# Kernel optimization log

Hardware: AMD Instinct MI355X
Metric: run time of the kernel (lower is better)

Reference implementation:

```python
import jax, jax.numpy as jnp
import numpy as np

REF_MIC = 0
LOAD = 0.001 / np.sqrt(2.0)  # diagonal loading added to both real and imag parts


def _to_complex(x):
    # x: (N, 2, ...) real/imag stacked -> complex (N, ...)
    return x[:, 0] + 1j * x[:, 1]


def setup_inputs() -> dict:
    key = jax.random.key(0)
    k1, k2, k3 = jax.random.split(key, 3)
    N, C, T, F = 8, 16, 300, 257
    mixture = jax.random.normal(k1, (N, 2, C, T, F), dtype=jnp.float32)
    target = jax.random.normal(k2, (N, 2, C, T, F), dtype=jnp.float32)
    steering_vector = jax.random.normal(k3, (N, 2, C, F), dtype=jnp.float32)
    return {"mixture": mixture, "target": target, "steering_vector": steering_vector}


def reference(mixture, target, steering_vector):
    N, _, C, T, F = mixture.shape
    y = _to_complex(mixture)  # (N, C, T, F)
    x = _to_complex(target)   # (N, C, T, F)

    # Spatial covariance of mixture, mean over time frames (sum/T), fused einsum
    # phi[n,f] = (1/T) * sum_t y[n,:,t,f] y[n,:,t,f]^H  -> (N, F, C, C)
    phi = jnp.einsum('nctf,ndtf->nfcd', y, jnp.conj(y)) / T
    eye = jnp.eye(C, dtype=phi.dtype)
    # original adds load to BOTH real and imag diagonals (broadcast over RI dim)
    phi = phi + (LOAD + 1j * LOAD) * eye
    phi_inv = jnp.linalg.inv(phi)  # (N, F, C, C)

    # Cross covariance between mixture and reference-mic target
    A = jnp.transpose(y, (0, 3, 2, 1))            # (N, F, T, C)
    b = jnp.transpose(x[:, REF_MIC], (0, 2, 1))   # (N, F, T)
    mu_a = jnp.mean(A, axis=(0, 2), keepdims=True)  # mean over batch and time
    mu_b = jnp.mean(b, axis=(0, 2), keepdims=True)
    # mean over T of (A-mu_a)(b-mu_b)^H -> (N, F, C)
    phi_yx0 = jnp.mean((A - mu_a) * jnp.conj(b - mu_b)[..., None], axis=2)

    # MWF weights: w = phi_inv @ phi_yx0  -> (N, F, C)
    w = jnp.einsum('nfcd,nfd->nfc', phi_inv, phi_yx0)

    # Beamform: X_bf[n,t,f] = w[n,f]^H y[n,:,t,f]
    Xbf = jnp.einsum('nfc,nctf->ntf', jnp.conj(w), y)  # (N, T, F)

    # Back to real/imag stacked (N, 2, 1, T, F) matching torch output layout
    out = jnp.stack([Xbf.real, Xbf.imag], axis=1)[:, :, None]
    return out
```

## Files before the change

### kernel.cpp

```cpp
#include <hip/hip_runtime.h>

#define N_     8
#define C_     16
#define T_     300
#define F_     257
#define TF_    (T_*F_)
#define CTF_   (C_*TF_)
#define N2CTF_ (2*CTF_)

#define FT_    32
#define NFT_   9
#define TS_    5
#define RST_   35
#define SROWS_ 88
#define SCNT_  (SROWS_*RST_)
#define NTILE_ 10
#define PHIC_  (NTILE_*16)

#define MREC_  272

#define LOADC  7.0710678118654755e-04f

typedef float v2f __attribute__((ext_vector_type(2)));

__device__ __forceinline__ float2 cmul(float2 a, float2 b) {
  return make_float2(a.x*b.x - a.y*b.y, a.x*b.y + a.y*b.x);
}
__device__ __forceinline__ float2 cmulc(float2 a, float2 b) {
  return make_float2(a.x*b.x + a.y*b.y, a.y*b.x - a.x*b.y);
}
__device__ __forceinline__ float2 cdiv(float2 a, float2 b) {
  float inv = 1.0f / (b.x*b.x + b.y*b.y);
  return make_float2((a.x*b.x + a.y*b.y)*inv, (a.y*b.x - a.x*b.y)*inv);
}
__device__ __forceinline__ float2 cadd(float2 a, float2 b){ return make_float2(a.x+b.x, a.y+b.y); }
__device__ __forceinline__ float2 csub(float2 a, float2 b){ return make_float2(a.x-b.x, a.y-b.y); }

template<int TCH>
__global__ __launch_bounds__(320, 1) void k1_cov(const float* __restrict__ mix,
                                                 const float* __restrict__ tgt,
                                                 float2* __restrict__ phi_pf,
                                                 float2* __restrict__ syx_pf,
                                                 float2* __restrict__ sy_pf,
                                                 float2* __restrict__ sx_pf) {
  __shared__ v2f ys[SCNT_];
  v2f* phi_p = (v2f*)phi_pf;
  v2f* syx_p = (v2f*)syx_pf;
  v2f* sy_p  = (v2f*)sy_pf;
  v2f* sx_p  = (v2f*)sx_pf;
  const int tid = threadIdx.x;
  const int ft = blockIdx.x, tc = blockIdx.y, n = blockIdx.z;
  const int fbase = ft * FT_;
  const int t0 = tc * TCH;
  const int fl = tid & 31;
  const int g  = tid >> 5;
  int ti = 0, tj = g;
  while (tj > ti) { ++ti; tj -= ti; }
  const int c0 = ti * 4;
  const int d0 = tj * 4;
  const bool sThread = (tj == 0);
  const bool xg = (g < 5);

  const float* mixN = mix + n * N2CTF_;
  const float* tgtN = tgt + n * N2CTF_;

  const int ts_g   = g >> 1;
  const int c_base = (g & 1) * 8;
  const int row0   = ts_g * 16 + c_base;
  const int f_ld = min(fbase + fl, F_ - 1);
  const float* ybase = mixN + c_base * TF_ + f_ld;
  const float* xbase = tgtN + f_ld;

  v2f acc[4][4];
  #pragma unroll
  for (int i = 0; i < 4; ++i)
    #pragma unroll
    for (int j = 0; j < 4; ++j) acc[i][j] = (v2f){0.f, 0.f};
  v2f syx[4], sy[4], sx = (v2f){0.f, 0.f};
  #pragma unroll
  for (int i = 0; i < 4; ++i) { syx[i] = (v2f){0.f,0.f}; sy[i] = (v2f){0.f,0.f}; }

  float lr[9], li[9];
  {
    #pragma unroll
    for (int k = 0; k < 8; ++k) {
      const float* p = ybase + k * TF_ + (t0 + ts_g) * F_;
      lr[k] = p[0]; li[k] = p[CTF_];
    }
    if (xg) { const float* p = xbase + (t0 + g) * F_; lr[8] = p[0]; li[8] = p[CTF_]; }
    #pragma unroll
    for (int k = 0; k < 8; ++k)
      ys[(row0 + k) * RST_ + fl] = (v2f){lr[k], li[k]};
    if (xg) ys[(80 + g) * RST_ + fl] = (v2f){lr[8], li[8]};
  }

  constexpr int NS = TCH / TS_;
  for (int stg = 0; stg < NS; ++stg) {
    __syncthreads();
    const bool more = (stg + 1 < NS);
    if (more) {
      const int tS = t0 + (stg + 1) * TS_;
      #pragma unroll
      for (int k = 0; k < 8; ++k) {
        const float* p = ybase + k * TF_ + (tS + ts_g) * F_;
        lr[k] = p[0]; li[k] = p[CTF_];
      }
      if (xg) { const float* p = xbase + (tS + g) * F_; lr[8] = p[0]; li[8] = p[CTF_]; }
    }
    #pragma unroll
    for (int tl = 0; tl < TS_; ++tl) {
      const int rb = tl * 16;
      v2f a[4], bu[4], bv[4];
      #pragma unroll
      for (int i = 0; i < 4; ++i) a[i] = ys[(rb + c0 + i) * RST_ + fl];
      #pragma unroll
      for (int j = 0; j < 4; ++j) {
        v2f b = ys[(rb + d0 + j) * RST_ + fl];
        bu[j] = (v2f){b.x, -b.y};
        bv[j] = (v2f){b.y,  b.x};
      }
      #pragma unroll
      for (int i = 0; i < 4; ++i)
        #pragma unroll
        for (int j = 0; j < 4; ++j)
          acc[i][j] += a[i].x * bu[j] + a[i].y * bv[j];
      if (sThread) {
        v2f xv = ys[(80 + tl) * RST_ + fl];
        v2f xu = (v2f){xv.x, -xv.y};
        v2f xw = (v2f){xv.y,  xv.x};
        #pragma unroll
        for (int i = 0; i < 4; ++i) {
          syx[i] += a[i].x * xu + a[i].y * xw;
          sy[i]  += a[i];
        }
        if (g == 0) sx += xv;
      }
    }
    __syncthreads();
    if (more) {
      #pragma unroll
      for (int k = 0; k < 8; ++k)
        ys[(row0 + k) * RST_ + fl] = (v2f){lr[k], li[k]};
      if (xg) ys[(80 + g) * RST_ + fl] = (v2f){lr[8], li[8]};
    }
  }

  const int f = fbase + fl;
  if (f < F_) {
    const int tcn = tc * N_ + n;
    v2f* pb = phi_p + ((size_t)tcn * F_ + f) * PHIC_ + g * 16;
    #pragma unroll
    for (int i = 0; i < 4; ++i)
      #pragma unroll
      for (int j = 0; j < 4; ++j) pb[i * 4 + j] = acc[i][j];
    if (sThread) {
      v2f* s1 = syx_p + ((size_t)tcn * F_ + f) * C_ + c0;
      v2f* s2 = sy_p  + ((size_t)tcn * F_ + f) * C_ + c0;
      #pragma unroll
      for (int i = 0; i < 4; ++i) { s1[i] = syx[i]; s2[i] = sy[i]; }
      if (g == 0) sx_p[(size_t)tcn * F_ + f] = sx;
    }
  }
}

template<int TCP>
__global__ __launch_bounds__(256) void k2a_reduce(const float2* __restrict__ phi_p,
                                                  const float2* __restrict__ syx_p,
                                                  const float2* __restrict__ sy_p,
                                                  const float2* __restrict__ sx_p,
                                                  float2* __restrict__ Mg) {
  __shared__ float2 ld_sy[TCP * N_ * C_];
  __shared__ float2 ld_syx[TCP * C_];
  __shared__ float2 ld_sx[TCP * N_];
  __shared__ float2 muB_s, sxO_s;
  const int f = blockIdx.x, n = blockIdx.y;
  const int tid = threadIdx.x;
  const int i = tid >> 4, j = tid & 15;

  const int ti = i >> 2, tj = j >> 2, ci = i & 3, cj = j & 3;
  int gL, cell; bool cj_flip;
  if (ti >= tj) { gL = ti * (ti + 1) / 2 + tj; cell = ci * 4 + cj; cj_flip = false; }
  else          { gL = tj * (tj + 1) / 2 + ti; cell = cj * 4 + ci; cj_flip = true; }
  const int off = gL * 16 + cell;

  float2 s = make_float2(0.f, 0.f);
  for (int tc = 0; tc < TCP; ++tc) {
    float2 v = phi_p[((size_t)(tc * N_ + n) * F_ + f) * PHIC_ + off];
    s.x += v.x; s.y += v.y;
  }
  if (cj_flip) s.y = -s.y;
  if (i == j) { s.x += (float)T_ * LOADC; s.y += (float)T_ * LOADC; }

  for (int idx = tid; idx < TCP * N_ * C_; idx += 256) {
    int tcn = idx >> 4, c = idx & 15;
    ld_sy[idx] = sy_p[((size_t)tcn * F_ + f) * C_ + c];
  }
  for (int idx = tid; idx < TCP * C_; idx += 256) {
    int tc = idx >> 4, c = idx & 15;
    ld_syx[idx] = syx_p[((size_t)(tc * N_ + n) * F_ + f) * C_ + c];
  }
  for (int idx = tid; idx < TCP * N_; idx += 256) {
    ld_sx[idx] = sx_p[(size_t)idx * F_ + f];
  }
  __syncthreads();

  float2 muA_r = make_float2(0.f,0.f), ownY = make_float2(0.f,0.f), ownYX = make_float2(0.f,0.f);
  if (tid < 16) {
    float2 allY = make_float2(0.f,0.f);
    for (int tcn = 0; tcn < TCP * N_; ++tcn) allY = cadd(allY, ld_sy[tcn * C_ + tid]);
    for (int tc = 0; tc < TCP; ++tc) {
      ownY  = cadd(ownY,  ld_sy[(tc * N_ + n) * C_ + tid]);
      ownYX = cadd(ownYX, ld_syx[tc * C_ + tid]);
    }
    const float invNT = 1.0f / ((float)N_ * (float)T_);
    muA_r = make_float2(allY.x * invNT, allY.y * invNT);
  }
  if (tid == 16) {
    float2 own = make_float2(0.f,0.f), all = make_float2(0.f,0.f);
    for (int tc = 0; tc < TCP; ++tc)
      for (int nn = 0; nn < N_; ++nn) {
        float2 v = ld_sx[tc * N_ + nn];
        all = cadd(all, v);
        if (nn == n) own = cadd(own, v);
      }
    const float invNT = 1.0f / ((float)N_ * (float)T_);
    muB_s = make_float2(all.x * invNT, all.y * invNT);
    sxO_s = own;
  }
  __syncthreads();

  float2* dst = Mg + (size_t)(n * F_ + f) * MREC_;
  dst[tid] = s;
  if (tid < 16) {
    float2 r = ownYX;
    r = csub(r, cmulc(muA_r, sxO_s));
    r = csub(r, cmulc(ownY, muB_s));
    float2 t3 = cmulc(muA_r, muB_s);
    r.x += (float)T_ * t3.x; r.y += (float)T_ * t3.y;
    dst[256 + tid] = r;
  }
}

__global__ __launch_bounds__(64) void k2b_solve(const float2* __restrict__ Mg,
                                                float* __restrict__ wre,
                                                float* __restrict__ wim) {
  __shared__ float2 M[16 * 17];
  const int f = blockIdx.x, n = blockIdx.y;
  const int tid = threadIdx.x;
  const float2* src = Mg + (size_t)(n * F_ + f) * MREC_;
  #pragma unroll
  for (int r = 0; r < 4; ++r) {
    int idx = tid + 64 * r;
    M[(idx >> 4) * 17 + (idx & 15)] = src[idx];
  }
  if (tid < 16) M[tid * 17 + 16] = src[256 + tid];
  __syncthreads();

  const int i = tid >> 2, q = tid & 3;
  for (int k = 0; k < 16; ++k) {
    float2 fac = cdiv(M[i * 17 + k], M[k * 17 + k]);
    __syncthreads();
    if (i != k) {
      #pragma unroll
      for (int jj = 0; jj < 4; ++jj) {
        int j = q * 4 + jj;
        M[i * 17 + j] = csub(M[i * 17 + j], cmul(fac, M[k * 17 + j]));
      }
      if (q == 3) M[i * 17 + 16] = csub(M[i * 17 + 16], cmul(fac, M[k * 17 + 16]));
    }
    __syncthreads();
  }
  if (q == 0) {
    float2 w = cdiv(M[i * 17 + 16], M[i * 17 + i]);
    wre[(n * C_ + i) * F_ + f] = w.x;
    wim[(n * C_ + i) * F_ + f] = w.y;
  }
}

__global__ __launch_bounds__(320) void k3_bf(const float* __restrict__ mix,
                                             const float* __restrict__ wre,
                                             const float* __restrict__ wim,
                                             float* __restrict__ out) {
  const int t0 = blockIdx.x * 2, n = blockIdx.y;
  const int f = threadIdx.x;
  if (f >= F_) return;
  const float* mixN = mix + n * N2CTF_;
  const float* wR = wre + n * C_ * F_;
  const float* wI = wim + n * C_ * F_;
  float* outN = out + n * 2 * TF_;
  float wr[16], wi[16];
  #pragma unroll
  for (int c = 0; c < 16; ++c) { wr[c] = wR[c * F_ + f]; wi[c] = wI[c * F_ + f]; }
  const float* yb = mixN + t0 * F_ + f;
  float xr0 = 0.f, xi0 = 0.f, xr1 = 0.f, xi1 = 0.f;
  #pragma unroll
  for (int c = 0; c < 16; ++c) {
    float yr0 = yb[c * TF_],      yi0 = yb[CTF_ + c * TF_];
    float yr1 = yb[c * TF_ + F_], yi1 = yb[CTF_ + c * TF_ + F_];
    xr0 += wr[c] * yr0 + wi[c] * yi0;
    xi0 += wr[c] * yi0 - wi[c] * yr0;
    xr1 += wr[c] * yr1 + wi[c] * yi1;
    xi1 += wr[c] * yi1 - wi[c] * yr1;
  }
  outN[t0 * F_ + f] = xr0;
  outN[TF_ + t0 * F_ + f] = xi0;
  outN[(t0 + 1) * F_ + f] = xr1;
  outN[TF_ + (t0 + 1) * F_ + f] = xi1;
}

template<int TCP>
static void launch_all(const float* mix, const float* tgt, float* ws, float* out,
                       hipStream_t stream) {
  constexpr int TCH = T_ / TCP;
  static_assert(TCH * TCP == T_ && TCH % TS_ == 0, "chunking");
  float2* phi_p = (float2*)ws;
  float2* syx_p = phi_p + (size_t)TCP * N_ * F_ * PHIC_;
  float2* sy_p  = syx_p + (size_t)TCP * N_ * F_ * C_;
  float2* sx_p  = sy_p  + (size_t)TCP * N_ * F_ * C_;
  float2* Mg    = sx_p  + (size_t)TCP * N_ * F_;
  float*  wre   = (float*)(Mg + (size_t)N_ * F_ * MREC_);
  float*  wim   = wre + N_ * C_ * F_;
  k1_cov<TCH><<<dim3(NFT_, TCP, N_), dim3(320), 0, stream>>>(mix, tgt, phi_p, syx_p, sy_p, sx_p);
  k2a_reduce<TCP><<<dim3(F_, N_), dim3(256), 0, stream>>>(phi_p, syx_p, sy_p, sx_p, Mg);
  k2b_solve<<<dim3(F_, N_), dim3(64), 0, stream>>>(Mg, wre, wim);
  k3_bf<<<dim3(T_ / 2, N_), dim3(320), 0, stream>>>(mix, wre, wim, out);
}

static size_t ws_need_bytes(int tcp) {
  size_t fl2 = (size_t)tcp * N_ * F_ * (PHIC_ + C_ + C_ + 1) + (size_t)N_ * F_ * MREC_;
  return fl2 * 8 + 2ull * N_ * C_ * F_ * 4;
}

extern "C" void kernel_launch(void* const* d_in, const int* in_sizes, int n_in,
                              void* d_out, int out_size, void* d_ws, size_t ws_size,
                              hipStream_t stream) {
  const float* mix = (const float*)d_in[0];
  const float* tgt = (const float*)d_in[1];
  float* out = (float*)d_out;
  float* ws  = (float*)d_ws;
  if (ws_size >= ws_need_bytes(12))      launch_all<12>(mix, tgt, ws, out, stream);
  else if (ws_size >= ws_need_bytes(10)) launch_all<10>(mix, tgt, ws, out, stream);
  else if (ws_size >= ws_need_bytes(6))  launch_all<6>(mix, tgt, ws, out, stream);
  else if (ws_size >= ws_need_bytes(2))  launch_all<2>(mix, tgt, ws, out, stream);
  else                                   launch_all<1>(mix, tgt, ws, out, stream);
}
```

Before: 237.9 us.

## Stage covariance inputs via direct global-to-LDS loads with double buffering

The covariance kernel now fills shared memory with `global_load_lds` DMA loads instead of loading into registers and writing them back. The shared buffer becomes a double-buffered, planar real/imag layout: one wave stages one time frame and the next stage is prefetched while the current one is computed, which removes one barrier per stage. Register pressure and LDS store instructions go down, and the min-blocks launch bound is relaxed. The 12-chunk time split is dropped in favour of at most 10, which shrinks the partial reduction but reduces parallelism in that kernel. Correctness depends on the compiler waiting for the async LDS loads before each barrier.

Measured after the change: 220.9 us. -7.1%, faster.

```diff
diff --git a/kernel.cpp b/kernel.cpp
--- a/kernel.cpp
+++ b/kernel.cpp
@@ -11,9 +11,9 @@
 #define FT_    32
 #define NFT_   9
 #define TS_    5
-#define RST_   35
-#define SROWS_ 88
-#define SCNT_  (SROWS_*RST_)
+#define SROW_  34
+#define SSTG_  (SROW_*32)
+#define SBUF_  (TS_*SSTG_)
 #define NTILE_ 10
 #define PHIC_  (NTILE_*16)
 
@@ -36,14 +36,20 @@
 __device__ __forceinline__ float2 cadd(float2 a, float2 b){ return make_float2(a.x+b.x, a.y+b.y); }
 __device__ __forceinline__ float2 csub(float2 a, float2 b){ return make_float2(a.x-b.x, a.y-b.y); }
 
+__device__ __forceinline__ void gload4(const float* g, float* l) {
+  __builtin_amdgcn_global_load_lds(
+      (const __attribute__((address_space(1))) unsigned int*)g,
+      (__attribute__((address_space(3))) unsigned int*)l, 4, 0, 0);
+}
+
 template<int TCH>
-__global__ __launch_bounds__(320, 1) void k1_cov(const float* __restrict__ mix,
-                                                 const float* __restrict__ tgt,
-                                                 float2* __restrict__ phi_pf,
-                                                 float2* __restrict__ syx_pf,
-                                                 float2* __restrict__ sy_pf,
-                                                 float2* __restrict__ sx_pf) {
-  __shared__ v2f ys[SCNT_];
+__global__ __launch_bounds__(320) void k1_cov(const float* __restrict__ mix,
+                                              const float* __restrict__ tgt,
+                                              float2* __restrict__ phi_pf,
+                                              float2* __restrict__ syx_pf,
+                                              float2* __restrict__ sy_pf,
+                                              float2* __restrict__ sx_pf) {
+  __shared__ float ys[2 * SBUF_];
   v2f* phi_p = (v2f*)phi_pf;
   v2f* syx_p = (v2f*)syx_pf;
   v2f* sy_p  = (v2f*)sy_pf;
@@ -59,17 +65,15 @@
   const int c0 = ti * 4;
   const int d0 = tj * 4;
   const bool sThread = (tj == 0);
-  const bool xg = (g < 5);
+
+  const int w     = tid >> 6;
+  const int plane = (tid >> 5) & 1;
+  const int f_ld  = min(fbase + fl, F_ - 1);
 
   const float* mixN = mix + n * N2CTF_;
   const float* tgtN = tgt + n * N2CTF_;
-
-  const int ts_g   = g >> 1;
-  const int c_base = (g & 1) * 8;
-  const int row0   = ts_g * 16 + c_base;
-  const int f_ld = min(fbase + fl, F_ - 1);
-  const float* ybase = mixN + c_base * TF_ + f_ld;
-  const float* xbase = tgtN + f_ld;
+  const float* ysrc = mixN + plane * CTF_ + (t0 + w) * F_ + f_ld;
+  const float* xsrc = tgtN + plane * CTF_ + (t0 + w) * F_ + f_ld;
 
   v2f acc[4][4];
   #pragma unroll
@@ -80,44 +84,41 @@
   #pragma unroll
   for (int i = 0; i < 4; ++i) { syx[i] = (v2f){0.f,0.f}; sy[i] = (v2f){0.f,0.f}; }
 
-  float lr[9], li[9];
+  constexpr int NS = TCH / TS_;
+
   {
+    float* dst = &ys[w * SSTG_];
     #pragma unroll
-    for (int k = 0; k < 8; ++k) {
-      const float* p = ybase + k * TF_ + (t0 + ts_g) * F_;
-      lr[k] = p[0]; li[k] = p[CTF_];
-    }
-    if (xg) { const float* p = xbase + (t0 + g) * F_; lr[8] = p[0]; li[8] = p[CTF_]; }
-    #pragma unroll
-    for (int k = 0; k < 8; ++k)
-      ys[(row0 + k) * RST_ + fl] = (v2f){lr[k], li[k]};
-    if (xg) ys[(80 + g) * RST_ + fl] = (v2f){lr[8], li[8]};
-  }
-
-  constexpr int NS = TCH / TS_;
-  for (int stg = 0; stg < NS; ++stg) {
+    for (int c = 0; c < 16; ++c) gload4(ysrc + c * TF_, dst + 2 * c * 32);
+    gload4(xsrc, dst + 32 * 32);
+  }
+
+  for (int s = 0; s < NS; ++s) {
     __syncthreads();
-    const bool more = (stg + 1 < NS);
-    if (more) {
-      const int tS = t0 + (stg + 1) * TS_;
-      #pragma unroll
-      for (int k = 0; k < 8; ++k) {
-        const float* p = ybase + k * TF_ + (tS + ts_g) * F_;
-        lr[k] = p[0]; li[k] = p[CTF_];
-      }
-      if (xg) { const float* p = xbase + (tS + g) * F_; lr[8] = p[0]; li[8] = p[CTF_]; }
-    }
+    if (s + 1 < NS) {
+      float* dst = &ys[((s + 1) & 1) * SBUF_ + w * SSTG_];
+      const float* yp = ysrc + (s + 1) * (TS_ * F_);
+      #pragma unroll
+      for (int c = 0; c < 16; ++c) gload4(yp + c * TF_, dst + 2 * c * 32);
+      gload4(xsrc + (s + 1) * (TS_ * F_), dst + 32 * 32);
+    }
+    const float* bufc = &ys[(s & 1) * SBUF_];
     #pragma unroll
     for (int tl = 0; tl < TS_; ++tl) {
-      const int rb = tl * 16;
+      const float* rt = bufc + tl * SSTG_;
       v2f a[4], bu[4], bv[4];
       #pragma unroll
-      for (int i = 0; i < 4; ++i) a[i] = ys[(rb + c0 + i) * RST_ + fl];
+      for (int i = 0; i < 4; ++i) {
+        float re = rt[(2 * (c0 + i)) * 32 + fl];
+        float im = rt[(2 * (c0 + i)) * 32 + 32 + fl];
+        a[i] = (v2f){re, im};
+      }
       #pragma unroll
       for (int j = 0; j < 4; ++j) {
-        v2f b = ys[(rb + d0 + j) * RST_ + fl];
-        bu[j] = (v2f){b.x, -b.y};
-        bv[j] = (v2f){b.y,  b.x};
+        float re = rt[(2 * (d0 + j)) * 32 + fl];
+        float im = rt[(2 * (d0 + j)) * 32 + 32 + fl];
+        bu[j] = (v2f){re, -im};
+        bv[j] = (v2f){im,  re};
       }
       #pragma unroll
       for (int i = 0; i < 4; ++i)
@@ -125,23 +126,17 @@
         for (int j = 0; j < 4; ++j)
           acc[i][j] += a[i].x * bu[j] + a[i].y * bv[j];
       if (sThread) {
-        v2f xv = ys[(80 + tl) * RST_ + fl];
-        v2f xu = (v2f){xv.x, -xv.y};
-        v2f xw = (v2f){xv.y,  xv.x};
+        float xre = rt[32 * 32 + fl];
+        float xim = rt[33 * 32 + fl];
+        v2f xu = (v2f){xre, -xim};
+        v2f xw = (v2f){xim,  xre};
         #pragma unroll
         for (int i = 0; i < 4; ++i) {
           syx[i] += a[i].x * xu + a[i].y * xw;
           sy[i]  += a[i];
         }
-        if (g == 0) sx += xv;
-      }
-    }
-    __syncthreads();
-    if (more) {
-      #pragma unroll
-      for (int k = 0; k < 8; ++k)
-        ys[(row0 + k) * RST_ + fl] = (v2f){lr[k], li[k]};
-      if (xg) ys[(80 + g) * RST_ + fl] = (v2f){lr[8], li[8]};
+        if (g == 0) sx += (v2f){xre, xim};
+      }
     }
   }
 
@@ -338,8 +333,7 @@
   const float* tgt = (const float*)d_in[1];
   float* out = (float*)d_out;
   float* ws  = (float*)d_ws;
-  if (ws_size >= ws_need_bytes(12))      launch_all<12>(mix, tgt, ws, out, stream);
-  else if (ws_size >= ws_need_bytes(10)) launch_all<10>(mix, tgt, ws, out, stream);
+  if (ws_size >= ws_need_bytes(10))      launch_all<10>(mix, tgt, ws, out, stream);
   else if (ws_size >= ws_need_bytes(6))  launch_all<6>(mix, tgt, ws, out, stream);
   else if (ws_size >= ws_need_bytes(2))  launch_all<2>(mix, tgt, ws, out, stream);
   else                                   launch_all<1>(mix, tgt, ws, out, stream);
```
